# Kernel optimization log

Hardware: AMD Instinct MI355X
Metric: run time of the kernel (lower is better)

## Reference

```python
import jax, jax.numpy as jnp
import numpy as np

N = 50000      # nodes
E = 1_600_000  # edges
IN, H, H2, OUT = 256, 128, 64, 2
EPS = 1e-5     # BatchNorm eps


def setup_inputs() -> dict:
    key = jax.random.key(0)
    ks = jax.random.split(key, 18)
    inp = {
        "x": jax.random.normal(ks[0], (N, IN), dtype=jnp.float32),
        "edge_index": jax.random.randint(ks[1], (2, E), 0, N, dtype=jnp.int64),
        # GCNConv 1
        "W1": jax.random.normal(ks[2], (IN, H), dtype=jnp.float32) / np.sqrt(IN),
        "b1": jnp.zeros((H,), dtype=jnp.float32),
        "g1": jnp.ones((H,), dtype=jnp.float32),
        "be1": jnp.zeros((H,), dtype=jnp.float32),
        "m1": jax.random.normal(ks[3], (H,), dtype=jnp.float32) * 0.1,
        "v1": jax.random.uniform(ks[4], (H,), dtype=jnp.float32, minval=0.5, maxval=1.5),
        # GCNConv 2
        "W2": jax.random.normal(ks[5], (H, H2), dtype=jnp.float32) / np.sqrt(H),
        "b2": jnp.zeros((H2,), dtype=jnp.float32),
        "g2": jnp.ones((H2,), dtype=jnp.float32),
        "be2": jnp.zeros((H2,), dtype=jnp.float32),
        "m2": jax.random.normal(ks[6], (H2,), dtype=jnp.float32) * 0.1,
        "v2": jax.random.uniform(ks[7], (H2,), dtype=jnp.float32, minval=0.5, maxval=1.5),
        # final linear
        "Wl": jax.random.normal(ks[8], (H2, OUT), dtype=jnp.float32) / np.sqrt(H2),
        "bl": jnp.zeros((OUT,), dtype=jnp.float32),
    }
    return inp


def _gcn_conv(x, W, b, src, dst, n_nodes):
    # PyG GCNConv: linear transform, then symmetric-normalized aggregation
    # with self-loops (gcn_norm, improved=False, fill_value=1).
    xw = x @ W                                            # [N, H]
    ones = jnp.ones((src.shape[0],), dtype=x.dtype)
    deg = jax.ops.segment_sum(ones, dst, num_segments=n_nodes) + 1.0  # +1 self-loop
    dinv = jax.lax.rsqrt(deg)                             # deg^{-1/2}
    norm = dinv[src] * dinv[dst]                          # [E]
    msgs = xw[src] * norm[:, None]                        # [E, H] gather
    agg = jax.ops.segment_sum(msgs, dst, num_segments=n_nodes)  # scatter-add
    agg = agg + xw * (1.0 / deg)[:, None]                 # self-loop term
    return agg + b


def _bn_relu(x, gamma, beta, mean, var):
    # inference-mode BatchNorm1d + ReLU
    xhat = (x - mean) * jax.lax.rsqrt(var + EPS)
    return jax.nn.relu(xhat * gamma + beta)


def reference(x, edge_index, W1, b1, g1, be1, m1, v1,
              W2, b2, g2, be2, m2, v2, Wl, bl):
    src, dst = edge_index[0], edge_index[1]
    h = _gcn_conv(x, W1, b1, src, dst, N)
    h = _bn_relu(h, g1, be1, m1, v1)
    # dropout is identity in eval mode
    h = _gcn_conv(h, W2, b2, src, dst, N)
    h = _bn_relu(h, g2, be2, m2, v2)
    return h @ Wl + bl
```

## Files before the change

kernel.cpp:

```cpp
#include <hip/hip_runtime.h>

#define N_NODES 50000
#define N_EDGES 1600000
#define IN_F 256
#define H1_F 128
#define H2_F 64
#define OUT_F 2
#define BN_EPS 1e-5f

#define NBUK 782
#define BCAP 3584
#define CHUNK 8192
#define NCHUNK 196

typedef __attribute__((ext_vector_type(8))) short bf16x8;
typedef __attribute__((ext_vector_type(4))) float f32x4;

__device__ __forceinline__ unsigned short f2b(float f) {
    union { float f; unsigned u; } v; v.f = f;
    unsigned r = (v.u + 0x7FFFu + ((v.u >> 16) & 1u)) >> 16;
    return (unsigned short)r;
}
__device__ __forceinline__ float b2f(unsigned short b) {
    union { unsigned u; float f; } v; v.u = ((unsigned)b) << 16;
    return v.f;
}
__device__ __forceinline__ void add2(float& a0, float& a1, unsigned u) {
    union { unsigned u; float f; } lo, hi;
    lo.u = u << 16;
    hi.u = u & 0xFFFF0000u;
    a0 += lo.f; a1 += hi.f;
}

__launch_bounds__(512)
__global__ void chist_kernel(const int* __restrict__ dst, int* __restrict__ h) {
    __shared__ int lh[NBUK];
    const int c = blockIdx.x;
    for (int i = threadIdx.x; i < NBUK; i += 512) lh[i] = 0;
    __syncthreads();
    const int e0 = c * CHUNK;
    const int e1 = min(e0 + CHUNK, N_EDGES);
    for (int e = e0 + threadIdx.x; e < e1; e += 512)
        atomicAdd(&lh[dst[e] >> 6], 1);
    __syncthreads();
    for (int i = threadIdx.x; i < NBUK; i += 512)
        h[c * NBUK + i] = lh[i];
}

__global__ void bscan2_kernel(int* __restrict__ h, int* __restrict__ boff,
                              int* __restrict__ rowptr) {
    __shared__ int tmp[1024];
    const int t = threadIdx.x;
    int tot = 0;
    if (t < NBUK)
        for (int c = 0; c < NCHUNK; ++c) tot += h[c * NBUK + t];
    tmp[t] = tot;
    __syncthreads();
    for (int off = 1; off < 1024; off <<= 1) {
        int a = (t >= off) ? tmp[t - off] : 0;
        __syncthreads();
        tmp[t] += a;
        __syncthreads();
    }
    const int excl = tmp[t] - tot;
    if (t < NBUK) boff[t] = excl;
    if (t == 0) { boff[NBUK] = N_EDGES; rowptr[N_NODES] = N_EDGES; }
    if (t < NBUK) {
        int run = excl;
        for (int c = 0; c < NCHUNK; ++c) {
            int v = h[c * NBUK + t];
            h[c * NBUK + t] = run;
            run += v;
        }
    }
}

__launch_bounds__(512)
__global__ void cscatter_kernel(const int* __restrict__ src, const int* __restrict__ dst,
                                const int* __restrict__ h, unsigned* __restrict__ bedges) {
    __shared__ int cur[NBUK];
    const int c = blockIdx.x;
    for (int i = threadIdx.x; i < NBUK; i += 512) cur[i] = h[c * NBUK + i];
    __syncthreads();
    const int e0 = c * CHUNK;
    const int e1 = min(e0 + CHUNK, N_EDGES);
    for (int e = e0 + threadIdx.x; e < e1; e += 512) {
        int s = src[e];
        int d = dst[e];
        int slot = atomicAdd(&cur[d >> 6], 1);
        bedges[slot] = (unsigned)s | ((unsigned)d << 16);
    }
}

__launch_bounds__(256)
__global__ void build_kernel(const unsigned* __restrict__ bedges, const int* __restrict__ boff,
                             unsigned short* __restrict__ perm, int* __restrict__ rowptr,
                             float* __restrict__ dinv) {
    __shared__ unsigned e_lds[BCAP];
    __shared__ unsigned short p_lds[BCAP];
    __shared__ int ncnt[64], ncur[64];

    const int b = blockIdx.x;
    const int t = threadIdx.x;
    const int start = boff[b];
    const int end   = boff[b + 1];
    const int cnt   = end - start;
    const bool fits = (cnt <= BCAP);

    if (t < 64) ncnt[t] = 0;
    __syncthreads();

    for (int i = t; i < cnt; i += 256) {
        unsigned e = bedges[start + i];
        if (fits) e_lds[i] = e;
        atomicAdd(&ncnt[(e >> 16) & 63], 1);
    }
    __syncthreads();

    if (t == 0) {
        int a = 0;
        for (int i = 0; i < 64; ++i) { ncur[i] = a; a += ncnt[i]; }
    }
    __syncthreads();

    if (t < 64) {
        int node = b * 64 + t;
        if (node < N_NODES) {
            rowptr[node] = start + ncur[t];
            dinv[node]   = rsqrtf((float)ncnt[t] + 1.0f);
        }
    }
    __syncthreads();

    for (int i = t; i < cnt; i += 256) {
        unsigned e = fits ? e_lds[i] : bedges[start + i];
        int slot = atomicAdd(&ncur[(e >> 16) & 63], 1);
        unsigned short s = (unsigned short)(e & 0xFFFFu);
        if (fits) p_lds[slot] = s;
        else      perm[start + slot] = s;
    }
    if (fits) {
        __syncthreads();
        for (int i = t; i < cnt; i += 256) perm[start + i] = p_lds[i];
    }
}

__global__ void wt_kernel(const float* __restrict__ W, unsigned short* __restrict__ WT,
                          int K, int N) {
    int i = blockIdx.x * blockDim.x + threadIdx.x;
    if (i < N * K) {
        int n = i / K, k = i % K;
        WT[i] = f2b(W[(size_t)k * N + n]);
    }
}

template <int KSTEPS, int NTILES, bool A_BF16>
__launch_bounds__(256)
__global__ void mfma_gemm_kernel(const void* __restrict__ Ap, const unsigned short* __restrict__ BT,
                                 const float* __restrict__ dscale, unsigned short* __restrict__ C,
                                 int M) {
    constexpr int K  = KSTEPS * 32;
    constexpr int NF = NTILES * 16;
    const int wave = threadIdx.x >> 6;
    const int lane = threadIdx.x & 63;
    const int r0   = (blockIdx.x * 4 + wave) * 16;
    const int m    = lane & 15;
    const int kb   = lane >> 4;

    int arow = r0 + m;
    if (arow >= M) arow = M - 1;

    f32x4 acc[NTILES];
#pragma unroll
    for (int nt = 0; nt < NTILES; ++nt) acc[nt] = (f32x4)(0.f);

#pragma unroll
    for (int ks = 0; ks < KSTEPS; ++ks) {
        const int k0 = ks * 32 + kb * 8;
        bf16x8 a;
        if constexpr (A_BF16) {
            a = *(const bf16x8*)((const unsigned short*)Ap + (size_t)arow * K + k0);
        } else {
            const float* af = (const float*)Ap + (size_t)arow * K + k0;
            float4 lo = *(const float4*)af;
            float4 hi = *(const float4*)(af + 4);
            union { bf16x8 v; unsigned short u[8]; } pk;
            pk.u[0] = f2b(lo.x); pk.u[1] = f2b(lo.y); pk.u[2] = f2b(lo.z); pk.u[3] = f2b(lo.w);
            pk.u[4] = f2b(hi.x); pk.u[5] = f2b(hi.y); pk.u[6] = f2b(hi.z); pk.u[7] = f2b(hi.w);
            a = pk.v;
        }
#pragma unroll
        for (int nt = 0; nt < NTILES; ++nt) {
            bf16x8 b = *(const bf16x8*)(BT + (size_t)(nt * 16 + m) * K + k0);
            acc[nt] = __builtin_amdgcn_mfma_f32_16x16x32_bf16(a, b, acc[nt], 0, 0, 0);
        }
    }

#pragma unroll
    for (int reg = 0; reg < 4; ++reg) {
        const int r = r0 + kb * 4 + reg;
        if (r < M) {
            const float ds = dscale[r];
#pragma unroll
            for (int nt = 0; nt < NTILES; ++nt)
                C[(size_t)r * NF + nt * 16 + m] = f2b(acc[nt][reg] * ds);
        }
    }
}

template <int HF, bool FINAL>
__launch_bounds__(256)
__global__ void agg_kernel(const int* __restrict__ rowptr, const unsigned short* __restrict__ perm,
                           const unsigned short* __restrict__ xwb, const float* __restrict__ dinv,
                           const float* __restrict__ bias, const float* __restrict__ g,
                           const float* __restrict__ be, const float* __restrict__ m,
                           const float* __restrict__ v, const float* __restrict__ Wl,
                           const float* __restrict__ bl, void* __restrict__ outp) {
    constexpr int FPQ = HF / 32;
    const int wid = (blockIdx.x * blockDim.x + threadIdx.x) >> 6;
    if (wid >= N_NODES) return;
    const int lane = threadIdx.x & 63;
    const int half = lane >> 5;
    const int l5   = lane & 31;
    const int f0   = l5 * FPQ;
    const int d    = wid;

    float acc[FPQ];
#pragma unroll
    for (int q = 0; q < FPQ; ++q) acc[q] = 0.f;

    if (half == 0) {
        if constexpr (FPQ == 4) {
            uint2 t = *(const uint2*)(xwb + (size_t)d * HF + f0);
            add2(acc[0], acc[1], t.x);
            add2(acc[2], acc[3], t.y);
        } else {
            unsigned t = *(const unsigned*)(xwb + (size_t)d * HF + f0);
            add2(acc[0], acc[1], t);
        }
    }

    const int start = rowptr[d];
    const int end   = rowptr[d + 1];
    for (int base = start; base < end; base += 64) {
        int pidx = base + lane;
        int pv = perm[pidx < end ? pidx : end - 1];
        int ne = end - base;
        if (ne > 64) ne = 64;
        if (ne == 64) {
#pragma unroll
            for (int j = 0; j < 64; j += 2) {
                int s = __shfl(pv, j + half);
                if constexpr (FPQ == 4) {
                    uint2 t = *(const uint2*)(xwb + (size_t)s * HF + f0);
                    add2(acc[0], acc[1], t.x);
                    add2(acc[2], acc[3], t.y);
                } else {
                    unsigned t = *(const unsigned*)(xwb + (size_t)s * HF + f0);
                    add2(acc[0], acc[1], t);
                }
            }
        } else {
            for (int j = 0; j < ne; j += 2) {
                int s = __shfl(pv, j + half);
                if (j + half < ne) {
                    if constexpr (FPQ == 4) {
                        uint2 t = *(const uint2*)(xwb + (size_t)s * HF + f0);
                        add2(acc[0], acc[1], t.x);
                        add2(acc[2], acc[3], t.y);
                    } else {
                        unsigned t = *(const unsigned*)(xwb + (size_t)s * HF + f0);
                        add2(acc[0], acc[1], t);
                    }
                }
            }
        }
    }

#pragma unroll
    for (int q = 0; q < FPQ; ++q) acc[q] += __shfl_xor(acc[q], 32);

    const float dv = dinv[d];
    float y[FPQ];
#pragma unroll
    for (int q = 0; q < FPQ; ++q) {
        int f = f0 + q;
        float s  = g[f] * rsqrtf(v[f] + BN_EPS);
        float sh = (bias[f] - m[f]) * s + be[f];
        y[q] = fmaxf(acc[q] * dv * s + sh, 0.f);
    }

    if constexpr (!FINAL) {
        if (half == 0) {
            if constexpr (FPQ == 4) {
                ushort4 o;
                o.x = f2b(y[0]); o.y = f2b(y[1]); o.z = f2b(y[2]); o.w = f2b(y[3]);
                *(ushort4*)((unsigned short*)outp + (size_t)d * HF + f0) = o;
            }
        }
    } else {
        float p0 = y[0] * Wl[f0 * 2 + 0] + y[1] * Wl[(f0 + 1) * 2 + 0];
        float p1 = y[0] * Wl[f0 * 2 + 1] + y[1] * Wl[(f0 + 1) * 2 + 1];
#pragma unroll
        for (int off = 16; off > 0; off >>= 1) {
            p0 += __shfl_xor(p0, off);
            p1 += __shfl_xor(p1, off);
        }
        if (lane == 0) {
            float* o = (float*)outp;
            o[(size_t)d * 2 + 0] = p0 + bl[0];
            o[(size_t)d * 2 + 1] = p1 + bl[1];
        }
    }
}

extern "C" void kernel_launch(void* const* d_in, const int* in_sizes, int n_in,
                              void* d_out, int out_size, void* d_ws, size_t ws_size,
                              hipStream_t stream) {
    const float* x   = (const float*)d_in[0];
    const int*   ei  = (const int*)d_in[1];
    const float* W1  = (const float*)d_in[2];
    const float* b1  = (const float*)d_in[3];
    const float* g1  = (const float*)d_in[4];
    const float* be1 = (const float*)d_in[5];
    const float* m1  = (const float*)d_in[6];
    const float* v1  = (const float*)d_in[7];
    const float* W2  = (const float*)d_in[8];
    const float* b2  = (const float*)d_in[9];
    const float* g2  = (const float*)d_in[10];
    const float* be2 = (const float*)d_in[11];
    const float* m2  = (const float*)d_in[12];
    const float* v2  = (const float*)d_in[13];
    const float* Wl  = (const float*)d_in[14];
    const float* bl  = (const float*)d_in[15];

    const int* src = ei;
    const int* dst = ei + N_EDGES;

    int*            h      = (int*)d_ws;
    int*            boff   = h + NCHUNK * NBUK;
    int*            rowptr = boff + 1024;
    float*          dinv   = (float*)(rowptr + 50016);
    unsigned*       bedges = (unsigned*)(dinv + 50016);
    unsigned short* perm   = (unsigned short*)(bedges + N_EDGES);
    unsigned short* xwb    = perm + N_EDGES;
    unsigned short* h1b    = xwb + (size_t)N_NODES * H1_F;
    unsigned short* w1t    = h1b + (size_t)N_NODES * H1_F;
    unsigned short* w2t    = w1t + H1_F * IN_F;

    chist_kernel<<<NCHUNK, 512, 0, stream>>>(dst, h);
    bscan2_kernel<<<1, 1024, 0, stream>>>(h, boff, rowptr);
    cscatter_kernel<<<NCHUNK, 512, 0, stream>>>(src, dst, h, bedges);
    build_kernel<<<NBUK, 256, 0, stream>>>(bedges, boff, perm, rowptr, dinv);

    wt_kernel<<<(H1_F * IN_F + 255) / 256, 256, 0, stream>>>(W1, w1t, IN_F, H1_F);
    wt_kernel<<<(H2_F * H1_F + 255) / 256, 256, 0, stream>>>(W2, w2t, H1_F, H2_F);

    mfma_gemm_kernel<IN_F / 32, H1_F / 16, false><<<(N_NODES + 63) / 64, 256, 0, stream>>>(
        x, w1t, dinv, xwb, N_NODES);
    agg_kernel<H1_F, false><<<(N_NODES * 64) / 256, 256, 0, stream>>>(
        rowptr, perm, xwb, dinv, b1, g1, be1, m1, v1, nullptr, nullptr, h1b);

    mfma_gemm_kernel<H1_F / 32, H2_F / 16, true><<<(N_NODES + 63) / 64, 256, 0, stream>>>(
        h1b, w2t, dinv, xwb, N_NODES);
    agg_kernel<H2_F, true><<<(N_NODES * 64) / 256, 256, 0, stream>>>(
        rowptr, perm, xwb, dinv, b2, g2, be2, m2, v2, Wl, bl, (float*)d_out);
}
```

Measured before the change: 254.4 us.

## Store features in 32-wide column chunks and split aggregation per chunk

```diff
diff --git a/kernel.cpp b/kernel.cpp
--- a/kernel.cpp
+++ b/kernel.cpp
@@ -12,9 +12,11 @@
 #define BCAP 3584
 #define CHUNK 8192
 #define NCHUNK 196
+#define FC 32
 
 typedef __attribute__((ext_vector_type(8))) short bf16x8;
 typedef __attribute__((ext_vector_type(4))) float f32x4;
+typedef __attribute__((ext_vector_type(4))) int   i32x4;
 
 __device__ __forceinline__ unsigned short f2b(float f) {
     union { float f; unsigned u; } v; v.f = f;
@@ -40,8 +42,15 @@
     __syncthreads();
     const int e0 = c * CHUNK;
     const int e1 = min(e0 + CHUNK, N_EDGES);
-    for (int e = e0 + threadIdx.x; e < e1; e += 512)
-        atomicAdd(&lh[dst[e] >> 6], 1);
+    const i32x4* p = (const i32x4*)(dst + e0);
+    const int n4 = (e1 - e0) >> 2;
+    for (int i = threadIdx.x; i < n4; i += 512) {
+        i32x4 d = __builtin_nontemporal_load(p + i);
+        atomicAdd(&lh[d.x >> 6], 1);
+        atomicAdd(&lh[d.y >> 6], 1);
+        atomicAdd(&lh[d.z >> 6], 1);
+        atomicAdd(&lh[d.w >> 6], 1);
+    }
     __syncthreads();
     for (int i = threadIdx.x; i < NBUK; i += 512)
         h[c * NBUK + i] = lh[i];
@@ -84,11 +93,17 @@
     __syncthreads();
     const int e0 = c * CHUNK;
     const int e1 = min(e0 + CHUNK, N_EDGES);
-    for (int e = e0 + threadIdx.x; e < e1; e += 512) {
-        int s = src[e];
-        int d = dst[e];
-        int slot = atomicAdd(&cur[d >> 6], 1);
-        bedges[slot] = (unsigned)s | ((unsigned)d << 16);
+    const i32x4* pd = (const i32x4*)(dst + e0);
+    const i32x4* ps = (const i32x4*)(src + e0);
+    const int n4 = (e1 - e0) >> 2;
+    for (int i = threadIdx.x; i < n4; i += 512) {
+        i32x4 d = __builtin_nontemporal_load(pd + i);
+        i32x4 s = __builtin_nontemporal_load(ps + i);
+        int slot;
+        slot = atomicAdd(&cur[d.x >> 6], 1); bedges[slot] = (unsigned)s.x | ((unsigned)d.x << 16);
+        slot = atomicAdd(&cur[d.y >> 6], 1); bedges[slot] = (unsigned)s.y | ((unsigned)d.y << 16);
+        slot = atomicAdd(&cur[d.z >> 6], 1); bedges[slot] = (unsigned)s.z | ((unsigned)d.z << 16);
+        slot = atomicAdd(&cur[d.w >> 6], 1); bedges[slot] = (unsigned)s.w | ((unsigned)d.w << 16);
     }
 }
 
@@ -154,13 +169,12 @@
     }
 }
 
-template <int KSTEPS, int NTILES, bool A_BF16>
+template <int KSTEPS, int NTILES, bool A_BF16_CHUNKED>
 __launch_bounds__(256)
 __global__ void mfma_gemm_kernel(const void* __restrict__ Ap, const unsigned short* __restrict__ BT,
                                  const float* __restrict__ dscale, unsigned short* __restrict__ C,
                                  int M) {
     constexpr int K  = KSTEPS * 32;
-    constexpr int NF = NTILES * 16;
     const int wave = threadIdx.x >> 6;
     const int lane = threadIdx.x & 63;
     const int r0   = (blockIdx.x * 4 + wave) * 16;
@@ -178,12 +192,13 @@
     for (int ks = 0; ks < KSTEPS; ++ks) {
         const int k0 = ks * 32 + kb * 8;
         bf16x8 a;
-        if constexpr (A_BF16) {
-            a = *(const bf16x8*)((const unsigned short*)Ap + (size_t)arow * K + k0);
+        if constexpr (A_BF16_CHUNKED) {
+            a = *(const bf16x8*)((const unsigned short*)Ap +
+                                 (size_t)ks * N_NODES * FC + (size_t)arow * FC + kb * 8);
         } else {
             const float* af = (const float*)Ap + (size_t)arow * K + k0;
-            float4 lo = *(const float4*)af;
-            float4 hi = *(const float4*)(af + 4);
+            f32x4 lo = __builtin_nontemporal_load((const f32x4*)af);
+            f32x4 hi = __builtin_nontemporal_load((const f32x4*)(af + 4));
             union { bf16x8 v; unsigned short u[8]; } pk;
             pk.u[0] = f2b(lo.x); pk.u[1] = f2b(lo.y); pk.u[2] = f2b(lo.z); pk.u[3] = f2b(lo.w);
             pk.u[4] = f2b(hi.x); pk.u[5] = f2b(hi.y); pk.u[6] = f2b(hi.z); pk.u[7] = f2b(hi.w);
@@ -202,116 +217,102 @@
         if (r < M) {
             const float ds = dscale[r];
 #pragma unroll
-            for (int nt = 0; nt < NTILES; ++nt)
-                C[(size_t)r * NF + nt * 16 + m] = f2b(acc[nt][reg] * ds);
-        }
-    }
-}
-
-template <int HF, bool FINAL>
+            for (int nt = 0; nt < NTILES; ++nt) {
+                C[(size_t)(nt >> 1) * N_NODES * FC + (size_t)r * FC + ((nt & 1) << 4) + m] =
+                    f2b(acc[nt][reg] * ds);
+            }
+        }
+    }
+}
+
 __launch_bounds__(256)
 __global__ void agg_kernel(const int* __restrict__ rowptr, const unsigned short* __restrict__ perm,
-                           const unsigned short* __restrict__ xwb, const float* __restrict__ dinv,
+                           const unsigned short* __restrict__ xw,
+                           const float* __restrict__ dinv,
                            const float* __restrict__ bias, const float* __restrict__ g,
                            const float* __restrict__ be, const float* __restrict__ m,
-                           const float* __restrict__ v, const float* __restrict__ Wl,
-                           const float* __restrict__ bl, void* __restrict__ outp) {
-    constexpr int FPQ = HF / 32;
-    const int wid = (blockIdx.x * blockDim.x + threadIdx.x) >> 6;
-    if (wid >= N_NODES) return;
+                           const float* __restrict__ v,
+                           unsigned short* __restrict__ out) {
+    const int c = blockIdx.y;
+    const unsigned short* xc = xw + (size_t)c * N_NODES * FC;
+    const int wave = threadIdx.x >> 6;
+    const int node = blockIdx.x * 4 + wave;
+    if (node >= N_NODES) return;
     const int lane = threadIdx.x & 63;
-    const int half = lane >> 5;
-    const int l5   = lane & 31;
-    const int f0   = l5 * FPQ;
-    const int d    = wid;
-
-    float acc[FPQ];
-#pragma unroll
-    for (int q = 0; q < FPQ; ++q) acc[q] = 0.f;
-
-    if (half == 0) {
-        if constexpr (FPQ == 4) {
-            uint2 t = *(const uint2*)(xwb + (size_t)d * HF + f0);
-            add2(acc[0], acc[1], t.x);
-            add2(acc[2], acc[3], t.y);
-        } else {
-            unsigned t = *(const unsigned*)(xwb + (size_t)d * HF + f0);
-            add2(acc[0], acc[1], t);
-        }
-    }
-
-    const int start = rowptr[d];
-    const int end   = rowptr[d + 1];
+    const int grp  = lane >> 4;
+    const int fp   = (lane & 15) << 1;
+
+    float a0 = 0.f, a1 = 0.f;
+    if (grp == 0) {
+        unsigned u = *(const unsigned*)(xc + node * FC + fp);
+        add2(a0, a1, u);
+    }
+
+    const int start = rowptr[node];
+    const int end   = rowptr[node + 1];
     for (int base = start; base < end; base += 64) {
         int pidx = base + lane;
-        int pv = perm[pidx < end ? pidx : end - 1];
+        int pv = (int)__builtin_nontemporal_load(perm + (pidx < end ? pidx : end - 1));
         int ne = end - base;
         if (ne > 64) ne = 64;
         if (ne == 64) {
 #pragma unroll
-            for (int j = 0; j < 64; j += 2) {
-                int s = __shfl(pv, j + half);
-                if constexpr (FPQ == 4) {
-                    uint2 t = *(const uint2*)(xwb + (size_t)s * HF + f0);
-                    add2(acc[0], acc[1], t.x);
-                    add2(acc[2], acc[3], t.y);
-                } else {
-                    unsigned t = *(const unsigned*)(xwb + (size_t)s * HF + f0);
-                    add2(acc[0], acc[1], t);
+            for (int j = 0; j < 64; j += 4) {
+                int s = __shfl(pv, j + grp);
+                unsigned u = *(const unsigned*)(xc + s * FC + fp);
+                add2(a0, a1, u);
+            }
+        } else {
+            for (int j = 0; j < ne; j += 4) {
+                int s = __shfl(pv, j + grp);
+                if (j + grp < ne) {
+                    unsigned u = *(const unsigned*)(xc + s * FC + fp);
+                    add2(a0, a1, u);
                 }
             }
-        } else {
-            for (int j = 0; j < ne; j += 2) {
-                int s = __shfl(pv, j + half);
-                if (j + half < ne) {
-                    if constexpr (FPQ == 4) {
-                        uint2 t = *(const uint2*)(xwb + (size_t)s * HF + f0);
-                        add2(acc[0], acc[1], t.x);
-                        add2(acc[2], acc[3], t.y);
-                    } else {
-                        unsigned t = *(const unsigned*)(xwb + (size_t)s * HF + f0);
-                        add2(acc[0], acc[1], t);
-                    }
-                }
-            }
-        }
-    }
-
-#pragma unroll
-    for (int q = 0; q < FPQ; ++q) acc[q] += __shfl_xor(acc[q], 32);
-
-    const float dv = dinv[d];
-    float y[FPQ];
-#pragma unroll
-    for (int q = 0; q < FPQ; ++q) {
-        int f = f0 + q;
-        float s  = g[f] * rsqrtf(v[f] + BN_EPS);
-        float sh = (bias[f] - m[f]) * s + be[f];
-        y[q] = fmaxf(acc[q] * dv * s + sh, 0.f);
-    }
-
-    if constexpr (!FINAL) {
-        if (half == 0) {
-            if constexpr (FPQ == 4) {
-                ushort4 o;
-                o.x = f2b(y[0]); o.y = f2b(y[1]); o.z = f2b(y[2]); o.w = f2b(y[3]);
-                *(ushort4*)((unsigned short*)outp + (size_t)d * HF + f0) = o;
-            }
-        }
-    } else {
-        float p0 = y[0] * Wl[f0 * 2 + 0] + y[1] * Wl[(f0 + 1) * 2 + 0];
-        float p1 = y[0] * Wl[f0 * 2 + 1] + y[1] * Wl[(f0 + 1) * 2 + 1];
-#pragma unroll
-        for (int off = 16; off > 0; off >>= 1) {
-            p0 += __shfl_xor(p0, off);
-            p1 += __shfl_xor(p1, off);
-        }
-        if (lane == 0) {
-            float* o = (float*)outp;
-            o[(size_t)d * 2 + 0] = p0 + bl[0];
-            o[(size_t)d * 2 + 1] = p1 + bl[1];
-        }
-    }
+        }
+    }
+
+    a0 += __shfl_xor(a0, 16); a1 += __shfl_xor(a1, 16);
+    a0 += __shfl_xor(a0, 32); a1 += __shfl_xor(a1, 32);
+
+    if (lane < 16) {
+        const float dv = dinv[node];
+        const int f = c * FC + fp;
+        float s0  = g[f] * rsqrtf(v[f] + BN_EPS);
+        float s1  = g[f + 1] * rsqrtf(v[f + 1] + BN_EPS);
+        float sh0 = (bias[f] - m[f]) * s0 + be[f];
+        float sh1 = (bias[f + 1] - m[f + 1]) * s1 + be[f + 1];
+        float y0 = fmaxf(a0 * dv * s0 + sh0, 0.f);
+        float y1 = fmaxf(a1 * dv * s1 + sh1, 0.f);
+        unsigned o = (unsigned)f2b(y0) | ((unsigned)f2b(y1) << 16);
+        __builtin_nontemporal_store(o, (unsigned*)(out + (size_t)c * N_NODES * FC + node * FC + fp));
+    }
+}
+
+__global__ void final_kernel(const unsigned short* __restrict__ h2, const float* __restrict__ Wl,
+                             const float* __restrict__ bl, float* __restrict__ out) {
+    __shared__ float w[H2_F * OUT_F];
+    if (threadIdx.x < H2_F * OUT_F) w[threadIdx.x] = Wl[threadIdx.x];
+    __syncthreads();
+    const int i = blockIdx.x * blockDim.x + threadIdx.x;
+    if (i >= N_NODES) return;
+    float p0 = bl[0], p1 = bl[1];
+#pragma unroll
+    for (int cc = 0; cc < 2; ++cc) {
+        const unsigned* p = (const unsigned*)(h2 + (size_t)cc * N_NODES * FC + i * FC);
+#pragma unroll
+        for (int q = 0; q < 16; ++q) {
+            unsigned t = p[q];
+            int f = cc * FC + q * 2;
+            float y0 = b2f((unsigned short)(t & 0xFFFF));
+            float y1 = b2f((unsigned short)(t >> 16));
+            p0 += y0 * w[f * 2 + 0] + y1 * w[(f + 1) * 2 + 0];
+            p1 += y0 * w[f * 2 + 1] + y1 * w[(f + 1) * 2 + 1];
+        }
+    }
+    out[(size_t)i * 2 + 0] = p0;
+    out[(size_t)i * 2 + 1] = p1;
 }
 
 extern "C" void kernel_launch(void* const* d_in, const int* in_sizes, int n_in,
@@ -358,11 +359,13 @@
 
     mfma_gemm_kernel<IN_F / 32, H1_F / 16, false><<<(N_NODES + 63) / 64, 256, 0, stream>>>(
         x, w1t, dinv, xwb, N_NODES);
-    agg_kernel<H1_F, false><<<(N_NODES * 64) / 256, 256, 0, stream>>>(
-        rowptr, perm, xwb, dinv, b1, g1, be1, m1, v1, nullptr, nullptr, h1b);
+    agg_kernel<<<dim3((N_NODES + 3) / 4, H1_F / FC), 256, 0, stream>>>(
+        rowptr, perm, xwb, dinv, b1, g1, be1, m1, v1, h1b);
 
     mfma_gemm_kernel<H1_F / 32, H2_F / 16, true><<<(N_NODES + 63) / 64, 256, 0, stream>>>(
         h1b, w2t, dinv, xwb, N_NODES);
-    agg_kernel<H2_F, true><<<(N_NODES * 64) / 256, 256, 0, stream>>>(
-        rowptr, perm, xwb, dinv, b2, g2, be2, m2, v2, Wl, bl, (float*)d_out);
-}
+    agg_kernel<<<dim3((N_NODES + 3) / 4, H2_F / FC), 256, 0, stream>>>(
+        rowptr, perm, xwb, dinv, b2, g2, be2, m2, v2, h1b);
+
+    final_kernel<<<(N_NODES + 255) / 256, 256, 0, stream>>>(h1b, Wl, bl, (float*)d_out);
+}
```

Result: slower. 332.7 us (+30.8%).
